# Kernel tuning notes

Measured on AMD Instinct MI355X. Metric: run time of the kernel, lower is better.

The kernel has to match this reference:

```python
import jax, jax.numpy as jnp
import numpy as np

N_DET, N_MAP, N_PTS, C = 900, 100, 20, 256
IMG_W, IMG_H = 640.0, 480.0


def _grid_sample(feat, gx, gy):
    """Bilinear grid_sample, align_corners=False, zeros padding.
    feat: [C,H,W]; gx,gy: [N] normalized in [-1,1]. Returns [N,C]."""
    Cc, H, W = feat.shape
    x = (gx + 1.0) * (W * 0.5) - 0.5
    y = (gy + 1.0) * (H * 0.5) - 0.5
    x0 = jnp.floor(x); y0 = jnp.floor(y)
    wx1 = x - x0; wx0 = 1.0 - wx1
    wy1 = y - y0; wy0 = 1.0 - wy1

    def gather(xi, yi):
        inb = (xi >= 0) & (xi <= W - 1) & (yi >= 0) & (yi <= H - 1)
        xc = jnp.clip(xi, 0, W - 1).astype(jnp.int32)
        yc = jnp.clip(yi, 0, H - 1).astype(jnp.int32)
        return feat[:, yc, xc] * inb.astype(feat.dtype)  # [C,N]

    out = (gather(x0, y0) * (wx0 * wy0) + gather(x0 + 1, y0) * (wx1 * wy0)
           + gather(x0, y0 + 1) * (wx0 * wy1) + gather(x0 + 1, y0 + 1) * (wx1 * wy1))
    return out.T  # [N,C]


def _project(E, K, homo):
    """E:[6,4,4], K:[6,3,3], homo:[N,4] -> gx,gy,valid each [6,N]."""
    pc = jnp.einsum('cij,nj->cni', E, homo)            # [6,N,4]
    p2d = jnp.einsum('cij,cnj->cni', K, pc[..., :3])   # [6,N,3]
    depth = p2d[..., 2]
    u = p2d[..., 0] / (depth + 1e-6)
    v = p2d[..., 1] / (depth + 1e-6)
    valid = depth > 0.1
    gx = u / IMG_W * 2.0 - 1.0
    gy = v / IMG_H * 2.0 - 1.0
    return gx, gy, valid


def _sample_multiscale(feats, gx, gy, valid):
    """feats: list of [6,C,H,W]; gx,gy,valid: [6,N] -> [6,N,C]."""
    acc = None
    for f in feats:  # fixed 4 FPN levels
        s = jax.vmap(_grid_sample)(f, gx, gy)  # [6,N,C]
        acc = s if acc is None else acc + s
    acc = acc / len(feats)
    return acc * valid[..., None].astype(acc.dtype)


def setup_inputs():
    key = jax.random.key(0)
    ks = jax.random.split(key, 16)
    f = lambda i, shape, s=1.0: jax.random.normal(ks[i], shape, jnp.float32) * s
    p2 = f(0, (6, C, 120, 160))
    p3 = f(1, (6, C, 60, 80))
    p4 = f(2, (6, C, 30, 40))
    p5 = f(3, (6, C, 15, 20))
    K0 = jnp.array([[500.0, 0.0, 320.0], [0.0, 500.0, 240.0], [0.0, 0.0, 1.0]], jnp.float32)
    intrinsics = jnp.tile(K0, (6, 1, 1)) + f(4, (6, 3, 3), 0.5)
    extrinsics = jnp.tile(jnp.eye(4, dtype=jnp.float32), (6, 1, 1)) + f(5, (6, 4, 4), 0.3)
    det_anchors_3d = f(6, (N_DET, 3), 20.0)
    det_anchors_full = f(7, (N_DET, 11))
    map_anchors = f(8, (N_MAP, N_PTS, 2), 20.0)
    s = 1.0 / float(np.sqrt(C))
    return {
        'p2': p2, 'p3': p3, 'p4': p4, 'p5': p5,
        'intrinsics': intrinsics, 'extrinsics': extrinsics,
        'det_anchors_3d': det_anchors_3d, 'det_anchors_full': det_anchors_full,
        'map_anchors': map_anchors,
        'W1d': f(9, (C, C), s), 'b1d': jnp.zeros((C,), jnp.float32),
        'Wcd': f(10, (C, 4), s), 'bcd': jnp.zeros((4,), jnp.float32),
        'Wod': f(11, (C, 11), s), 'bod': jnp.zeros((11,), jnp.float32),
        'W1m': f(12, (C, C), s), 'b1m': jnp.zeros((C,), jnp.float32),
        'Wcm': f(13, (C, 3), s), 'bcm': jnp.zeros((3,), jnp.float32),
        'Wom': f(14, (C, N_PTS * 2), s), 'bom': jnp.zeros((N_PTS * 2,), jnp.float32),
    }


def reference(p2, p3, p4, p5, intrinsics, extrinsics, det_anchors_3d,
              det_anchors_full, map_anchors, W1d, b1d, Wcd, bcd, Wod, bod,
              W1m, b1m, Wcm, bcm, Wom, bom):
    feats = [p2, p3, p4, p5]
    ones_det = jnp.ones((N_DET, 1), det_anchors_3d.dtype)
    homo_det = jnp.concatenate([det_anchors_3d, ones_det], axis=-1)  # [900,4]
    centers = map_anchors.mean(axis=1)  # [100,2]
    homo_map = jnp.concatenate([centers,
                                jnp.zeros((N_MAP, 1), centers.dtype),
                                jnp.ones((N_MAP, 1), centers.dtype)], axis=-1)  # [100,4]

    gxd, gyd, vd = _project(extrinsics, intrinsics, homo_det)
    det_agg = _sample_multiscale(feats, gxd, gyd, vd).sum(0) / 6.0  # [900,256]
    gxm, gym, vm = _project(extrinsics, intrinsics, homo_map)
    map_agg = _sample_multiscale(feats, gxm, gym, vm).sum(0) / 6.0  # [100,256]

    hd = jax.nn.relu(det_agg @ W1d + b1d)
    det_classes = hd @ Wcd + bcd                     # [900,4]
    det_boxes = det_anchors_full + hd @ Wod + bod    # [900,11]
    hm = jax.nn.relu(map_agg @ W1m + b1m)
    map_classes = hm @ Wcm + bcm                     # [100,3]
    map_lines = map_anchors + (hm @ Wom + bom).reshape(N_MAP, N_PTS, 2)
    return det_classes, det_boxes, map_classes, map_lines
```

## Files before the change

### kernel.cpp

```cpp
#include <hip/hip_runtime.h>

#define CDIM 256
#define NDET 900
#define NMAP 100
#define NPTS 20
#define NBLK (NDET + NMAP)

#define P4OFF 7372800
#define P5OFF 9216000
#define C3STR 1228800
#define C4STR 307200
#define C5STR 76800

__global__ __launch_bounds__(256) void t_pack(
    const float* __restrict__ p3, const float* __restrict__ p4,
    const float* __restrict__ p5, float* __restrict__ wsf)
{
    const int b = blockIdx.x;
    const int t = threadIdx.x;
    if (b < 360) {
        const int cam = b / 60, h = b % 60;
        const float4* __restrict__ src = (const float4*)(p3 + ((cam * CDIM + t) * 60 + h) * 80);
        float* __restrict__ dst = wsf + ((cam * 60 + h) * 80) * CDIM + t;
        #pragma unroll
        for (int w4 = 0; w4 < 20; ++w4) {
            const float4 v = src[w4];
            dst[(w4 * 4 + 0) * CDIM] = v.x;
            dst[(w4 * 4 + 1) * CDIM] = v.y;
            dst[(w4 * 4 + 2) * CDIM] = v.z;
            dst[(w4 * 4 + 3) * CDIM] = v.w;
        }
    } else if (b < 540) {
        const int bb = b - 360;
        const int cam = bb / 30, h = bb % 30;
        const float4* __restrict__ src = (const float4*)(p4 + ((cam * CDIM + t) * 30 + h) * 40);
        float* __restrict__ dst = wsf + P4OFF + ((cam * 30 + h) * 40) * CDIM + t;
        #pragma unroll
        for (int w4 = 0; w4 < 10; ++w4) {
            const float4 v = src[w4];
            dst[(w4 * 4 + 0) * CDIM] = v.x;
            dst[(w4 * 4 + 1) * CDIM] = v.y;
            dst[(w4 * 4 + 2) * CDIM] = v.z;
            dst[(w4 * 4 + 3) * CDIM] = v.w;
        }
    } else {
        const int bb = b - 540;
        const int cam = bb / 15, h = bb % 15;
        const float4* __restrict__ src = (const float4*)(p5 + ((cam * CDIM + t) * 15 + h) * 20);
        float* __restrict__ dst = wsf + P5OFF + ((cam * 15 + h) * 20) * CDIM + t;
        #pragma unroll
        for (int w4 = 0; w4 < 5; ++w4) {
            const float4 v = src[w4];
            dst[(w4 * 4 + 0) * CDIM] = v.x;
            dst[(w4 * 4 + 1) * CDIM] = v.y;
            dst[(w4 * 4 + 2) * CDIM] = v.z;
            dst[(w4 * 4 + 3) * CDIM] = v.w;
        }
    }
}

__global__ __launch_bounds__(256, 4) void autonav_fused(
    const float* __restrict__ p2, const float* __restrict__ wsf,
    const float* __restrict__ Kin, const float* __restrict__ Ein,
    const float* __restrict__ det3d, const float* __restrict__ detfull,
    const float* __restrict__ mapanch,
    const float* __restrict__ W1d, const float* __restrict__ b1d,
    const float* __restrict__ Wcd, const float* __restrict__ bcd,
    const float* __restrict__ Wod, const float* __restrict__ bod,
    const float* __restrict__ W1m, const float* __restrict__ b1m,
    const float* __restrict__ Wcm, const float* __restrict__ bcm,
    const float* __restrict__ Wom, const float* __restrict__ bom,
    float* __restrict__ out)
{
    const int pt = blockIdx.x;
    const int t  = threadIdx.x;
    const bool isDet = (pt < NDET);
    const int m = pt - NDET;

    __shared__ int   s_off[25][4];
    __shared__ float s_w[25][4];
    __shared__ int   s_list[32];
    __shared__ int   s_n;
    __shared__ float s_vec[CDIM];
    __shared__ float s_hid[CDIM];

    if (t < 25) {
        float h0, h1, h2;
        if (isDet) {
            h0 = det3d[pt * 3 + 0];
            h1 = det3d[pt * 3 + 1];
            h2 = det3d[pt * 3 + 2];
        } else {
            float cx = 0.f, cy = 0.f;
            #pragma unroll
            for (int j = 0; j < NPTS; ++j) {
                cx += mapanch[(m * NPTS + j) * 2 + 0];
                cy += mapanch[(m * NPTS + j) * 2 + 1];
            }
            h0 = cx / (float)NPTS;
            h1 = cy / (float)NPTS;
            h2 = 0.f;
        }

        bool pred = false;
        if (t < 24) {
            const int cam = t >> 2, l = t & 3;
            float pc[3];
            #pragma unroll
            for (int i = 0; i < 3; ++i) {
                pc[i] = Ein[cam * 16 + i * 4 + 0] * h0
                      + Ein[cam * 16 + i * 4 + 1] * h1
                      + Ein[cam * 16 + i * 4 + 2] * h2
                      + Ein[cam * 16 + i * 4 + 3] * 1.f;
            }
            const float q0 = Kin[cam*9+0]*pc[0] + Kin[cam*9+1]*pc[1] + Kin[cam*9+2]*pc[2];
            const float q1 = Kin[cam*9+3]*pc[0] + Kin[cam*9+4]*pc[1] + Kin[cam*9+5]*pc[2];
            const float q2 = Kin[cam*9+6]*pc[0] + Kin[cam*9+7]*pc[1] + Kin[cam*9+8]*pc[2];
            const float depth = q2;
            const float u = q0 / (depth + 1e-6f);
            const float v = q1 / (depth + 1e-6f);
            const bool valid = (depth > 0.1f);
            const float gx = u / 640.0f * 2.0f - 1.0f;
            const float gy = v / 480.0f * 2.0f - 1.0f;

            const int Hs[4] = {120, 60, 30, 15};
            const int Ws[4] = {160, 80, 40, 20};
            const int H = Hs[l], W = Ws[l];
            const float x = (gx + 1.f) * (W * 0.5f) - 0.5f;
            const float y = (gy + 1.f) * (H * 0.5f) - 0.5f;
            const float x0f = floorf(x), y0f = floorf(y);
            const float wx1 = x - x0f, wx0 = 1.f - wx1;
            const float wy1 = y - y0f, wy0 = 1.f - wy1;
            const float x1f = x0f + 1.f, y1f = y0f + 1.f;
            const bool bx0 = (x0f >= 0.f) && (x0f <= (float)(W - 1));
            const bool bx1 = (x1f >= 0.f) && (x1f <= (float)(W - 1));
            const bool by0 = (y0f >= 0.f) && (y0f <= (float)(H - 1));
            const bool by1 = (y1f >= 0.f) && (y1f <= (float)(H - 1));
            const int xc0 = (int)fminf(fmaxf(x0f, 0.f), (float)(W - 1));
            const int xc1 = (int)fminf(fmaxf(x1f, 0.f), (float)(W - 1));
            const int yc0 = (int)fminf(fmaxf(y0f, 0.f), (float)(H - 1));
            const int yc1 = (int)fminf(fmaxf(y1f, 0.f), (float)(H - 1));
            if (l == 0) {
                const int base = cam * CDIM * H * W;
                s_off[t][0] = base + yc0 * W + xc0;
                s_off[t][1] = base + yc0 * W + xc1;
                s_off[t][2] = base + yc1 * W + xc0;
                s_off[t][3] = base + yc1 * W + xc1;
            } else {
                const int pb = (l == 1) ? cam * C3STR
                             : (l == 2) ? (P4OFF + cam * C4STR)
                                        : (P5OFF + cam * C5STR);
                s_off[t][0] = pb + (yc0 * W + xc0) * CDIM;
                s_off[t][1] = pb + (yc0 * W + xc1) * CDIM;
                s_off[t][2] = pb + (yc1 * W + xc0) * CDIM;
                s_off[t][3] = pb + (yc1 * W + xc1) * CDIM;
            }
            const float w0 = (bx0 && by0) ? wx0 * wy0 : 0.f;
            const float w1 = (bx1 && by0) ? wx1 * wy0 : 0.f;
            const float w2 = (bx0 && by1) ? wx0 * wy1 : 0.f;
            const float w3 = (bx1 && by1) ? wx1 * wy1 : 0.f;
            s_w[t][0] = w0; s_w[t][1] = w1; s_w[t][2] = w2; s_w[t][3] = w3;
            pred = valid && ((w0 + w1 + w2 + w3) != 0.f);
        } else {
            s_off[24][0] = 0; s_off[24][1] = 0; s_off[24][2] = 0; s_off[24][3] = 0;
            s_w[24][0] = 0.f; s_w[24][1] = 0.f; s_w[24][2] = 0.f; s_w[24][3] = 0.f;
        }

        const unsigned long long mask = __ballot(pred);
        const int n = __popcll(mask);
        const int rank = __popcll(mask & ((1ull << t) - 1ull));
        if (pred) s_list[rank] = t;
        const int npad = (n + 7) & ~7;
        if (t < 8 && (n + t) < npad) s_list[n + t] = 24;
        if (t == 0) s_n = npad;
    }
    __syncthreads();

    float acc = 0.f;
    const int npad = s_n;
    for (int base = 0; base < npad; base += 8) {
        float v[8][4];
        int tj[8];
        #pragma unroll
        for (int j = 0; j < 8; ++j) {
            const int tt = s_list[base + j];
            tj[j] = tt;
            const bool isP2 = (tt < 24) && ((tt & 3) == 0);
            const float* f = isP2 ? p2 : wsf;
            const int coff = isP2 ? t * 19200 : t;
            v[j][0] = f[s_off[tt][0] + coff];
            v[j][1] = f[s_off[tt][1] + coff];
            v[j][2] = f[s_off[tt][2] + coff];
            v[j][3] = f[s_off[tt][3] + coff];
        }
        #pragma unroll
        for (int j = 0; j < 8; ++j) {
            const int tt = tj[j];
            acc += s_w[tt][0] * v[j][0] + s_w[tt][1] * v[j][1]
                 + s_w[tt][2] * v[j][2] + s_w[tt][3] * v[j][3];
        }
    }
    const float agg = (acc * 0.25f) / 6.0f;

    s_vec[t] = agg;
    __syncthreads();

    const float* __restrict__ W1 = isDet ? W1d : W1m;
    const float* __restrict__ b1 = isDet ? b1d : b1m;
    float hsum = b1[t];
    const float4* sv4 = (const float4*)s_vec;
    float wvA[32], wvB[32];
    #pragma unroll
    for (int i = 0; i < 32; ++i) wvA[i] = W1[i * CDIM + t];
    #pragma unroll
    for (int k0 = 0; k0 < CDIM; k0 += 64) {
        #pragma unroll
        for (int i = 0; i < 32; ++i) wvB[i] = W1[(k0 + 32 + i) * CDIM + t];
        #pragma unroll
        for (int i = 0; i < 8; ++i) {
            const float4 x = sv4[(k0 >> 2) + i];
            hsum = fmaf(x.x, wvA[4 * i + 0], hsum);
            hsum = fmaf(x.y, wvA[4 * i + 1], hsum);
            hsum = fmaf(x.z, wvA[4 * i + 2], hsum);
            hsum = fmaf(x.w, wvA[4 * i + 3], hsum);
        }
        if (k0 + 64 < CDIM) {
            #pragma unroll
            for (int i = 0; i < 32; ++i) wvA[i] = W1[(k0 + 64 + i) * CDIM + t];
        }
        #pragma unroll
        for (int i = 0; i < 8; ++i) {
            const float4 x = sv4[(k0 >> 2) + 8 + i];
            hsum = fmaf(x.x, wvB[4 * i + 0], hsum);
            hsum = fmaf(x.y, wvB[4 * i + 1], hsum);
            hsum = fmaf(x.z, wvB[4 * i + 2], hsum);
            hsum = fmaf(x.w, wvB[4 * i + 3], hsum);
        }
    }
    s_hid[t] = fmaxf(hsum, 0.f);
    __syncthreads();

    const int g  = t >> 4;
    const int ln = t & 15;
    const int nOut = isDet ? 15 : 43;
    const int nrep = isDet ? 1 : 3;
    for (int rep = 0; rep < nrep; ++rep) {
        const int o = g + rep * 16;
        if (o < nOut) {
            const float* Wp; int stride, oo, ooff; float bias;
            if (isDet) {
                if (o < 4) { Wp = Wcd; stride = 4;  oo = o;     ooff = pt * 4 + oo;         bias = bcd[oo]; }
                else       { Wp = Wod; stride = 11; oo = o - 4; ooff = 3600 + pt * 11 + oo; bias = bod[oo] + detfull[pt * 11 + oo]; }
            } else {
                if (o < 3) { Wp = Wcm; stride = 3;  oo = o;     ooff = 13500 + m * 3 + oo;  bias = bcm[oo]; }
                else       { Wp = Wom; stride = 40; oo = o - 3; ooff = 13800 + m * 40 + oo; bias = bom[oo] + mapanch[m * 40 + oo]; }
            }
            float wv[16], xv[16];
            #pragma unroll
            for (int kk = 0; kk < 16; ++kk) wv[kk] = Wp[(ln + kk * 16) * stride + oo];
            #pragma unroll
            for (int kk = 0; kk < 16; ++kk) xv[kk] = s_hid[ln + kk * 16];
            float sp = 0.f;
            #pragma unroll
            for (int kk = 0; kk < 16; ++kk) sp = fmaf(xv[kk], wv[kk], sp);
            #pragma unroll
            for (int off = 1; off < 16; off <<= 1) sp += __shfl_xor(sp, off, 64);
            if (ln == 0) out[ooff] = sp + bias;
        }
    }
}

extern "C" void kernel_launch(void* const* d_in, const int* in_sizes, int n_in,
                              void* d_out, int out_size, void* d_ws, size_t ws_size,
                              hipStream_t stream) {
    const float* p2      = (const float*)d_in[0];
    const float* p3      = (const float*)d_in[1];
    const float* p4      = (const float*)d_in[2];
    const float* p5      = (const float*)d_in[3];
    const float* Kin     = (const float*)d_in[4];
    const float* Ein     = (const float*)d_in[5];
    const float* det3d   = (const float*)d_in[6];
    const float* detfull = (const float*)d_in[7];
    const float* mapanch = (const float*)d_in[8];
    const float* W1d     = (const float*)d_in[9];
    const float* b1d     = (const float*)d_in[10];
    const float* Wcd     = (const float*)d_in[11];
    const float* bcd     = (const float*)d_in[12];
    const float* Wod     = (const float*)d_in[13];
    const float* bod     = (const float*)d_in[14];
    const float* W1m     = (const float*)d_in[15];
    const float* b1m     = (const float*)d_in[16];
    const float* Wcm     = (const float*)d_in[17];
    const float* bcm     = (const float*)d_in[18];
    const float* Wom     = (const float*)d_in[19];
    const float* bom     = (const float*)d_in[20];
    float* out = (float*)d_out;
    float* wsf = (float*)d_ws;

    t_pack<<<630, 256, 0, stream>>>(p3, p4, p5, wsf);

    autonav_fused<<<NBLK, 256, 0, stream>>>(
        p2, wsf, Kin, Ein, det3d, detfull, mapanch,
        W1d, b1d, Wcd, bcd, Wod, bod, W1m, b1m, Wcm, bcm, Wom, bom, out);
}
```

Baseline: 51.79 us.

## Move P2 level sampling into the pack kernel to overlap with transposes

The P2 bilinear gather for every query point, which reads the untransposed NCHW layout with strided loads, moves from the fused MLP kernel into extra blocks of the pack kernel. Those blocks run alongside the P3-P5 transpose blocks and write per-point partial sums to workspace. The second kernel starts from that partial sum and gathers only the three packed levels. This is meant to hide the slow P2 gathers behind the transpose work, at the cost of an extra workspace round trip, a second projection pass, and a larger first launch.

```diff
diff --git a/kernel.cpp b/kernel.cpp
--- a/kernel.cpp
+++ b/kernel.cpp
@@ -8,59 +8,179 @@
 
 #define P4OFF 7372800
 #define P5OFF 9216000
+#define ACCOFF 9292800
 #define C3STR 1228800
 #define C4STR 307200
 #define C5STR 76800
 
-__global__ __launch_bounds__(256) void t_pack(
-    const float* __restrict__ p3, const float* __restrict__ p4,
-    const float* __restrict__ p5, float* __restrict__ wsf)
+__global__ __launch_bounds__(256, 4) void k1_pack_p2(
+    const float* __restrict__ p2, const float* __restrict__ p3,
+    const float* __restrict__ p4, const float* __restrict__ p5,
+    const float* __restrict__ Kin, const float* __restrict__ Ein,
+    const float* __restrict__ det3d, const float* __restrict__ mapanch,
+    float* __restrict__ wsf)
 {
     const int b = blockIdx.x;
     const int t = threadIdx.x;
-    if (b < 360) {
-        const int cam = b / 60, h = b % 60;
-        const float4* __restrict__ src = (const float4*)(p3 + ((cam * CDIM + t) * 60 + h) * 80);
-        float* __restrict__ dst = wsf + ((cam * 60 + h) * 80) * CDIM + t;
-        #pragma unroll
-        for (int w4 = 0; w4 < 20; ++w4) {
-            const float4 v = src[w4];
-            dst[(w4 * 4 + 0) * CDIM] = v.x;
-            dst[(w4 * 4 + 1) * CDIM] = v.y;
-            dst[(w4 * 4 + 2) * CDIM] = v.z;
-            dst[(w4 * 4 + 3) * CDIM] = v.w;
-        }
-    } else if (b < 540) {
-        const int bb = b - 360;
-        const int cam = bb / 30, h = bb % 30;
-        const float4* __restrict__ src = (const float4*)(p4 + ((cam * CDIM + t) * 30 + h) * 40);
-        float* __restrict__ dst = wsf + P4OFF + ((cam * 30 + h) * 40) * CDIM + t;
-        #pragma unroll
-        for (int w4 = 0; w4 < 10; ++w4) {
-            const float4 v = src[w4];
-            dst[(w4 * 4 + 0) * CDIM] = v.x;
-            dst[(w4 * 4 + 1) * CDIM] = v.y;
-            dst[(w4 * 4 + 2) * CDIM] = v.z;
-            dst[(w4 * 4 + 3) * CDIM] = v.w;
-        }
-    } else {
-        const int bb = b - 540;
-        const int cam = bb / 15, h = bb % 15;
-        const float4* __restrict__ src = (const float4*)(p5 + ((cam * CDIM + t) * 15 + h) * 20);
-        float* __restrict__ dst = wsf + P5OFF + ((cam * 15 + h) * 20) * CDIM + t;
-        #pragma unroll
-        for (int w4 = 0; w4 < 5; ++w4) {
-            const float4 v = src[w4];
-            dst[(w4 * 4 + 0) * CDIM] = v.x;
-            dst[(w4 * 4 + 1) * CDIM] = v.y;
-            dst[(w4 * 4 + 2) * CDIM] = v.z;
-            dst[(w4 * 4 + 3) * CDIM] = v.w;
-        }
-    }
+
+    if (b < 630) {
+        if (b < 360) {
+            const int cam = b / 60, h = b % 60;
+            const float4* __restrict__ src = (const float4*)(p3 + ((cam * CDIM + t) * 60 + h) * 80);
+            float* __restrict__ dst = wsf + ((cam * 60 + h) * 80) * CDIM + t;
+            #pragma unroll
+            for (int w4 = 0; w4 < 20; ++w4) {
+                const float4 v = src[w4];
+                dst[(w4 * 4 + 0) * CDIM] = v.x;
+                dst[(w4 * 4 + 1) * CDIM] = v.y;
+                dst[(w4 * 4 + 2) * CDIM] = v.z;
+                dst[(w4 * 4 + 3) * CDIM] = v.w;
+            }
+        } else if (b < 540) {
+            const int bb = b - 360;
+            const int cam = bb / 30, h = bb % 30;
+            const float4* __restrict__ src = (const float4*)(p4 + ((cam * CDIM + t) * 30 + h) * 40);
+            float* __restrict__ dst = wsf + P4OFF + ((cam * 30 + h) * 40) * CDIM + t;
+            #pragma unroll
+            for (int w4 = 0; w4 < 10; ++w4) {
+                const float4 v = src[w4];
+                dst[(w4 * 4 + 0) * CDIM] = v.x;
+                dst[(w4 * 4 + 1) * CDIM] = v.y;
+                dst[(w4 * 4 + 2) * CDIM] = v.z;
+                dst[(w4 * 4 + 3) * CDIM] = v.w;
+            }
+        } else {
+            const int bb = b - 540;
+            const int cam = bb / 15, h = bb % 15;
+            const float4* __restrict__ src = (const float4*)(p5 + ((cam * CDIM + t) * 15 + h) * 20);
+            float* __restrict__ dst = wsf + P5OFF + ((cam * 15 + h) * 20) * CDIM + t;
+            #pragma unroll
+            for (int w4 = 0; w4 < 5; ++w4) {
+                const float4 v = src[w4];
+                dst[(w4 * 4 + 0) * CDIM] = v.x;
+                dst[(w4 * 4 + 1) * CDIM] = v.y;
+                dst[(w4 * 4 + 2) * CDIM] = v.z;
+                dst[(w4 * 4 + 3) * CDIM] = v.w;
+            }
+        }
+        return;
+    }
+
+    const int pt = b - 630;
+    const bool isDet = (pt < NDET);
+    const int m = pt - NDET;
+
+    __shared__ int   s_off0[7][4];
+    __shared__ float s_w0[7][4];
+    __shared__ int   s_list0[8];
+    __shared__ int   s_n0;
+
+    if (t < 7) {
+        float h0, h1, h2;
+        if (isDet) {
+            h0 = det3d[pt * 3 + 0];
+            h1 = det3d[pt * 3 + 1];
+            h2 = det3d[pt * 3 + 2];
+        } else {
+            float cx = 0.f, cy = 0.f;
+            #pragma unroll
+            for (int j = 0; j < NPTS; ++j) {
+                cx += mapanch[(m * NPTS + j) * 2 + 0];
+                cy += mapanch[(m * NPTS + j) * 2 + 1];
+            }
+            h0 = cx / (float)NPTS;
+            h1 = cy / (float)NPTS;
+            h2 = 0.f;
+        }
+
+        bool pred = false;
+        if (t < 6) {
+            const int cam = t;
+            float pc[3];
+            #pragma unroll
+            for (int i = 0; i < 3; ++i) {
+                pc[i] = Ein[cam * 16 + i * 4 + 0] * h0
+                      + Ein[cam * 16 + i * 4 + 1] * h1
+                      + Ein[cam * 16 + i * 4 + 2] * h2
+                      + Ein[cam * 16 + i * 4 + 3] * 1.f;
+            }
+            const float q0 = Kin[cam*9+0]*pc[0] + Kin[cam*9+1]*pc[1] + Kin[cam*9+2]*pc[2];
+            const float q1 = Kin[cam*9+3]*pc[0] + Kin[cam*9+4]*pc[1] + Kin[cam*9+5]*pc[2];
+            const float q2 = Kin[cam*9+6]*pc[0] + Kin[cam*9+7]*pc[1] + Kin[cam*9+8]*pc[2];
+            const float depth = q2;
+            const float u = q0 / (depth + 1e-6f);
+            const float v = q1 / (depth + 1e-6f);
+            const bool valid = (depth > 0.1f);
+            const float gx = u / 640.0f * 2.0f - 1.0f;
+            const float gy = v / 480.0f * 2.0f - 1.0f;
+
+            const int H = 120, W = 160;
+            const float x = (gx + 1.f) * (W * 0.5f) - 0.5f;
+            const float y = (gy + 1.f) * (H * 0.5f) - 0.5f;
+            const float x0f = floorf(x), y0f = floorf(y);
+            const float wx1 = x - x0f, wx0 = 1.f - wx1;
+            const float wy1 = y - y0f, wy0 = 1.f - wy1;
+            const float x1f = x0f + 1.f, y1f = y0f + 1.f;
+            const bool bx0 = (x0f >= 0.f) && (x0f <= (float)(W - 1));
+            const bool bx1 = (x1f >= 0.f) && (x1f <= (float)(W - 1));
+            const bool by0 = (y0f >= 0.f) && (y0f <= (float)(H - 1));
+            const bool by1 = (y1f >= 0.f) && (y1f <= (float)(H - 1));
+            const int xc0 = (int)fminf(fmaxf(x0f, 0.f), (float)(W - 1));
+            const int xc1 = (int)fminf(fmaxf(x1f, 0.f), (float)(W - 1));
+            const int yc0 = (int)fminf(fmaxf(y0f, 0.f), (float)(H - 1));
+            const int yc1 = (int)fminf(fmaxf(y1f, 0.f), (float)(H - 1));
+            const int base = cam * CDIM * H * W;
+            s_off0[t][0] = base + yc0 * W + xc0;
+            s_off0[t][1] = base + yc0 * W + xc1;
+            s_off0[t][2] = base + yc1 * W + xc0;
+            s_off0[t][3] = base + yc1 * W + xc1;
+            const float w0 = (bx0 && by0) ? wx0 * wy0 : 0.f;
+            const float w1 = (bx1 && by0) ? wx1 * wy0 : 0.f;
+            const float w2 = (bx0 && by1) ? wx0 * wy1 : 0.f;
+            const float w3 = (bx1 && by1) ? wx1 * wy1 : 0.f;
+            s_w0[t][0] = w0; s_w0[t][1] = w1; s_w0[t][2] = w2; s_w0[t][3] = w3;
+            pred = valid && ((w0 + w1 + w2 + w3) != 0.f);
+        } else {
+            s_off0[6][0] = 0; s_off0[6][1] = 0; s_off0[6][2] = 0; s_off0[6][3] = 0;
+            s_w0[6][0] = 0.f; s_w0[6][1] = 0.f; s_w0[6][2] = 0.f; s_w0[6][3] = 0.f;
+        }
+        const unsigned long long mask = __ballot(pred);
+        const int n = __popcll(mask);
+        const int rank = __popcll(mask & ((1ull << t) - 1ull));
+        if (pred) s_list0[rank] = t;
+        const int npad = (n + 1) & ~1;
+        if (t < 2 && (n + t) < npad) s_list0[n + t] = 6;
+        if (t == 0) s_n0 = npad;
+    }
+    __syncthreads();
+
+    float acc = 0.f;
+    const int npad = s_n0;
+    const int cHW = t * 19200;
+    for (int base = 0; base < npad; base += 2) {
+        float v[2][4];
+        int tj[2];
+        #pragma unroll
+        for (int j = 0; j < 2; ++j) {
+            const int tt = s_list0[base + j];
+            tj[j] = tt;
+            v[j][0] = p2[s_off0[tt][0] + cHW];
+            v[j][1] = p2[s_off0[tt][1] + cHW];
+            v[j][2] = p2[s_off0[tt][2] + cHW];
+            v[j][3] = p2[s_off0[tt][3] + cHW];
+        }
+        #pragma unroll
+        for (int j = 0; j < 2; ++j) {
+            const int tt = tj[j];
+            acc += s_w0[tt][0] * v[j][0] + s_w0[tt][1] * v[j][1]
+                 + s_w0[tt][2] * v[j][2] + s_w0[tt][3] * v[j][3];
+        }
+    }
+    wsf[ACCOFF + pt * CDIM + t] = acc;
 }
 
-__global__ __launch_bounds__(256, 4) void autonav_fused(
-    const float* __restrict__ p2, const float* __restrict__ wsf,
+__global__ __launch_bounds__(256, 4) void k2_gather_mlp(
+    const float* __restrict__ wsf,
     const float* __restrict__ Kin, const float* __restrict__ Ein,
     const float* __restrict__ det3d, const float* __restrict__ detfull,
     const float* __restrict__ mapanch,
@@ -77,14 +197,16 @@
     const bool isDet = (pt < NDET);
     const int m = pt - NDET;
 
-    __shared__ int   s_off[25][4];
-    __shared__ float s_w[25][4];
-    __shared__ int   s_list[32];
+    __shared__ int   s_off[19][4];
+    __shared__ float s_w[19][4];
+    __shared__ int   s_list[24];
     __shared__ int   s_n;
     __shared__ float s_vec[CDIM];
     __shared__ float s_hid[CDIM];
 
-    if (t < 25) {
+    float acc = wsf[ACCOFF + pt * CDIM + t];
+
+    if (t < 19) {
         float h0, h1, h2;
         if (isDet) {
             h0 = det3d[pt * 3 + 0];
@@ -103,8 +225,8 @@
         }
 
         bool pred = false;
-        if (t < 24) {
-            const int cam = t >> 2, l = t & 3;
+        if (t < 18) {
+            const int cam = t / 3, l = 1 + (t % 3);
             float pc[3];
             #pragma unroll
             for (int i = 0; i < 3; ++i) {
@@ -140,21 +262,13 @@
             const int xc1 = (int)fminf(fmaxf(x1f, 0.f), (float)(W - 1));
             const int yc0 = (int)fminf(fmaxf(y0f, 0.f), (float)(H - 1));
             const int yc1 = (int)fminf(fmaxf(y1f, 0.f), (float)(H - 1));
-            if (l == 0) {
-                const int base = cam * CDIM * H * W;
-                s_off[t][0] = base + yc0 * W + xc0;
-                s_off[t][1] = base + yc0 * W + xc1;
-                s_off[t][2] = base + yc1 * W + xc0;
-                s_off[t][3] = base + yc1 * W + xc1;
-            } else {
-                const int pb = (l == 1) ? cam * C3STR
-                             : (l == 2) ? (P4OFF + cam * C4STR)
-                                        : (P5OFF + cam * C5STR);
-                s_off[t][0] = pb + (yc0 * W + xc0) * CDIM;
-                s_off[t][1] = pb + (yc0 * W + xc1) * CDIM;
-                s_off[t][2] = pb + (yc1 * W + xc0) * CDIM;
-                s_off[t][3] = pb + (yc1 * W + xc1) * CDIM;
-            }
+            const int pb = (l == 1) ? cam * C3STR
+                         : (l == 2) ? (P4OFF + cam * C4STR)
+                                    : (P5OFF + cam * C5STR);
+            s_off[t][0] = pb + (yc0 * W + xc0) * CDIM;
+            s_off[t][1] = pb + (yc0 * W + xc1) * CDIM;
+            s_off[t][2] = pb + (yc1 * W + xc0) * CDIM;
+            s_off[t][3] = pb + (yc1 * W + xc1) * CDIM;
             const float w0 = (bx0 && by0) ? wx0 * wy0 : 0.f;
             const float w1 = (bx1 && by0) ? wx1 * wy0 : 0.f;
             const float w2 = (bx0 && by1) ? wx0 * wy1 : 0.f;
@@ -162,8 +276,8 @@
             s_w[t][0] = w0; s_w[t][1] = w1; s_w[t][2] = w2; s_w[t][3] = w3;
             pred = valid && ((w0 + w1 + w2 + w3) != 0.f);
         } else {
-            s_off[24][0] = 0; s_off[24][1] = 0; s_off[24][2] = 0; s_off[24][3] = 0;
-            s_w[24][0] = 0.f; s_w[24][1] = 0.f; s_w[24][2] = 0.f; s_w[24][3] = 0.f;
+            s_off[18][0] = 0; s_off[18][1] = 0; s_off[18][2] = 0; s_off[18][3] = 0;
+            s_w[18][0] = 0.f; s_w[18][1] = 0.f; s_w[18][2] = 0.f; s_w[18][3] = 0.f;
         }
 
         const unsigned long long mask = __ballot(pred);
@@ -171,12 +285,11 @@
         const int rank = __popcll(mask & ((1ull << t) - 1ull));
         if (pred) s_list[rank] = t;
         const int npad = (n + 7) & ~7;
-        if (t < 8 && (n + t) < npad) s_list[n + t] = 24;
+        if (t < 8 && (n + t) < npad) s_list[n + t] = 18;
         if (t == 0) s_n = npad;
     }
     __syncthreads();
 
-    float acc = 0.f;
     const int npad = s_n;
     for (int base = 0; base < npad; base += 8) {
         float v[8][4];
@@ -185,13 +298,10 @@
         for (int j = 0; j < 8; ++j) {
             const int tt = s_list[base + j];
             tj[j] = tt;
-            const bool isP2 = (tt < 24) && ((tt & 3) == 0);
-            const float* f = isP2 ? p2 : wsf;
-            const int coff = isP2 ? t * 19200 : t;
-            v[j][0] = f[s_off[tt][0] + coff];
-            v[j][1] = f[s_off[tt][1] + coff];
-            v[j][2] = f[s_off[tt][2] + coff];
-            v[j][3] = f[s_off[tt][3] + coff];
+            v[j][0] = wsf[s_off[tt][0] + t];
+            v[j][1] = wsf[s_off[tt][1] + t];
+            v[j][2] = wsf[s_off[tt][2] + t];
+            v[j][3] = wsf[s_off[tt][3] + t];
         }
         #pragma unroll
         for (int j = 0; j < 8; ++j) {
@@ -297,9 +407,10 @@
     float* out = (float*)d_out;
     float* wsf = (float*)d_ws;
 
-    t_pack<<<630, 256, 0, stream>>>(p3, p4, p5, wsf);
-
-    autonav_fused<<<NBLK, 256, 0, stream>>>(
-        p2, wsf, Kin, Ein, det3d, detfull, mapanch,
+    k1_pack_p2<<<1630, 256, 0, stream>>>(
+        p2, p3, p4, p5, Kin, Ein, det3d, mapanch, wsf);
+
+    k2_gather_mlp<<<NBLK, 256, 0, stream>>>(
+        wsf, Kin, Ein, det3d, detfull, mapanch,
         W1d, b1d, Wcd, bcd, Wod, bod, W1m, b1m, Wcm, bcm, Wom, bom, out);
 }
```

New measurement: 52.45 us. No clear change (+1.3%).
